# Performance work log

Hardware: AMD Instinct MI355X
Metric: run time of the kernel (lower is better)

The kernel has to match this reference:

```python
import jax, jax.numpy as jnp
import numpy as np

TOPOLOGY = [-1, 0, 0, 0, 1, 2, 3, 4, 5, 6, 7, 8, 9, 9, 9, 12, 13, 14, 16, 17, 18, 19, 20, 21]
JOINT_WEIGHTS = np.ones(24, dtype=np.float32)
B1 = 1.0
B2 = 1.0


def quaternion_to_matrix(q):
    # pytorch3d convention: real part first (w, x, y, z)
    w, x, y, z = q[..., 0], q[..., 1], q[..., 2], q[..., 3]
    two_s = 2.0 / jnp.sum(q * q, axis=-1)
    o = jnp.stack([
        1 - two_s * (y * y + z * z), two_s * (x * y - z * w), two_s * (x * z + y * w),
        two_s * (x * y + z * w), 1 - two_s * (x * x + z * z), two_s * (y * z - x * w),
        two_s * (x * z - y * w), two_s * (y * z + x * w), 1 - two_s * (x * x + y * y),
    ], axis=-1)
    return o.reshape(q.shape[:-1] + (3, 3))


def fk(topology, X_m, X_t):
    # X_m: (bs, T, J*4+3), X_t: (bs, J, 3)
    J = len(topology)
    quat = X_m[..., :-3].reshape(X_m.shape[:-1] + (J, 4))
    local_rot = quaternion_to_matrix(quat)          # (bs, T, J, 3, 3)
    grots = [None] * J
    gtrs = [None] * J
    grots[0] = local_rot[..., 0, :, :]
    gtrs[0] = X_m[..., -3:]                          # root translation
    for i in range(1, J):
        pi = topology[i]
        grots[i] = jnp.matmul(grots[pi], local_rot[..., i, :, :])
        gtrs[i] = jnp.einsum('btij,bj->bti', grots[pi], X_t[:, i]) + gtrs[pi]
    return jnp.stack(grots, axis=-3), jnp.stack(gtrs, axis=-2)


def split_raw_motion(raw_motion):
    position = raw_motion[..., -3:]
    rotation = raw_motion[..., :-3]
    rotation = rotation.reshape(rotation.shape[:-1] + (-1, 4))
    norm = jnp.linalg.norm(rotation, axis=-1, keepdims=True)
    rotation = rotation / jnp.maximum(norm, 1e-12)
    return rotation, position


def weighted_mse(w, a, b):
    # w: (J,), a/b: (bs, T, J, C) -> per-joint weighted mean squared error
    return jnp.mean(w[None, None, :, None] * (a - b) ** 2)


def setup_inputs() -> dict:
    key = jax.random.key(0)
    k1, k2, k3, k4 = jax.random.split(key, 4)
    bs, T, J = 64, 2048, 24
    return {
        'Y_m': jax.random.normal(k1, (bs, T, J * 4 + 3), dtype=jnp.float32),
        'X_m': jax.random.normal(k2, (bs, T, J * 4 + 3), dtype=jnp.float32),
        'Y_t': jax.random.normal(k3, (bs, J, 3), dtype=jnp.float32),
        'X_t': jax.random.normal(k4, (bs, J, 3), dtype=jnp.float32),
    }


def reference(Y_m, X_m, Y_t, X_t):
    w = jnp.asarray(JOINT_WEIGHTS)
    rot_x, pos_x = split_raw_motion(X_m)
    rot_y, pos_y = split_raw_motion(Y_m)
    grot_y, gtr_y = fk(TOPOLOGY, Y_m, Y_t)
    grot_x, gtr_x = fk(TOPOLOGY, X_m, X_t)
    loss_rot = B1 * weighted_mse(w, rot_y, rot_x)
    loss_fk = B2 * (2.5 * weighted_mse(w, gtr_y, gtr_x)
                    + jnp.mean((pos_y - pos_x) ** 2))
    return loss_rot + loss_fk
```

## Files before the change

### kernel.cpp

```cpp
#include <hip/hip_runtime.h>

#define BS 64
#define TT 2048
#define NJ 24
#define ROWF 99
#define BLOCK 64
#define NROWS (BS * TT)
#define LSTR 20

__device__ __forceinline__ float4 ld4u(const float* __restrict__ p) {
  return *reinterpret_cast<const float4*>(p);
}

__device__ __forceinline__ void quat2mat_s(float w, float x, float y, float z,
                                           float s, float* R) {
  const float xx = s*x*x, yy = s*y*y, zz = s*z*z;
  const float xy = s*x*y, xz = s*x*z, yz = s*y*z;
  const float xw = s*x*w, yw = s*y*w, zw = s*z*w;
  R[0] = 1.0f - (yy+zz); R[1] = xy - zw;        R[2] = xz + yw;
  R[3] = xy + zw;        R[4] = 1.0f - (xx+zz); R[5] = yz - xw;
  R[6] = xz - yw;        R[7] = yz + xw;        R[8] = 1.0f - (xx+yy);
}

__device__ __forceinline__ void mm3(const float* A, const float* B, float* C) {
#pragma unroll
  for (int r = 0; r < 3; ++r) {
#pragma unroll
    for (int c = 0; c < 3; ++c) {
      C[3*r+c] = fmaf(A[3*r], B[c], fmaf(A[3*r+1], B[3+c], A[3*r+2]*B[6+c]));
    }
  }
}

__global__ __launch_bounds__(BLOCK, 2) void motion_loss_kernel(
    const float* __restrict__ Ym, const float* __restrict__ Xm,
    const float* __restrict__ Yt, const float* __restrict__ Xt,
    float* __restrict__ out) {
  __shared__ __align__(16) float lX[2][BLOCK * LSTR];
  __shared__ __align__(16) float lY[2][BLOCK * LSTR];

  const int t = threadIdx.x;
  const size_t row0 = (size_t)blockIdx.x * BLOCK;
  const int b = blockIdx.x >> 5;
  const float* __restrict__ xt = Xm + row0 * ROWF;
  const float* __restrict__ yt = Ym + row0 * ROWF;
  const float* __restrict__ tX = Xt + (size_t)b * NJ * 3;
  const float* __restrict__ tY = Yt + (size_t)b * NJ * 3;

  const float4 posx = ld4u(xt + t * ROWF + 95);
  const float4 posy = ld4u(yt + t * ROWF + 95);

  float4 sx[4], sy[4];

#define STAGE_ISSUE(w) do {                                                    \
    _Pragma("unroll")                                                          \
    for (int k = 0; k < 4; ++k) {                                              \
      const int l = t + k * BLOCK, r = l >> 2, s = l & 3;                      \
      sx[k] = ld4u(xt + r * ROWF + (w) * 16 + s * 4);                          \
      sy[k] = ld4u(yt + r * ROWF + (w) * 16 + s * 4);                          \
    }                                                                          \
  } while (0)

#define STAGE_WRITE(w) do {                                                    \
    _Pragma("unroll")                                                          \
    for (int k = 0; k < 4; ++k) {                                              \
      const int l = t + k * BLOCK, r = l >> 2, s = l & 3;                      \
      *reinterpret_cast<float4*>(&lX[(w) & 1][r * LSTR + s * 4]) = sx[k];      \
      *reinterpret_cast<float4*>(&lY[(w) & 1][r * LSTR + s * 4]) = sy[k];      \
    }                                                                          \
  } while (0)

  STAGE_ISSUE(0);
  STAGE_WRITE(0);
  STAGE_ISSUE(1);

  float GX[3][9], GY[3][9], D[3][3];
  float rot_acc = 0.0f, gtr_acc = 0.0f, pos_acc = 0.0f;

  {
    const float4 vx = *reinterpret_cast<const float4*>(&lX[0][t * LSTR]);
    const float4 vy = *reinterpret_cast<const float4*>(&lY[0][t * LSTR]);
    const float qqx = vx.x*vx.x + vx.y*vx.y + vx.z*vx.z + vx.w*vx.w;
    const float qqy = vy.x*vy.x + vy.y*vy.y + vy.z*vy.z + vy.w*vy.w;
    const float ix = rsqrtf(fmaxf(qqx, 1e-24f));
    const float iy = rsqrtf(fmaxf(qqy, 1e-24f));
    const float r0 = vy.x*iy - vx.x*ix, r1 = vy.y*iy - vx.y*ix;
    const float r2 = vy.z*iy - vx.z*ix, r3 = vy.w*iy - vx.w*ix;
    rot_acc += r0*r0 + r1*r1 + r2*r2 + r3*r3;
    quat2mat_s(vx.x, vx.y, vx.z, vx.w, 2.0f*ix*ix, GX[0]);
    quat2mat_s(vy.x, vy.y, vy.z, vy.w, 2.0f*iy*iy, GY[0]);
    D[0][0] = posy.y - posx.y; D[0][1] = posy.z - posx.z; D[0][2] = posy.w - posx.w;
    const float dd = D[0][0]*D[0][0] + D[0][1]*D[0][1] + D[0][2]*D[0][2];
    gtr_acc += dd;
    pos_acc  = dd;
  }

#define JSTEP(j, PS, NS) do {                                                  \
    const float4 vx = *reinterpret_cast<const float4*>(                        \
        &lX[((j) >> 2) & 1][t * LSTR + ((j) & 3) * 4]);                        \
    const float4 vy = *reinterpret_cast<const float4*>(                        \
        &lY[((j) >> 2) & 1][t * LSTR + ((j) & 3) * 4]);                        \
    const float qqx = vx.x*vx.x + vx.y*vx.y + vx.z*vx.z + vx.w*vx.w;           \
    const float qqy = vy.x*vy.x + vy.y*vy.y + vy.z*vy.z + vy.w*vy.w;           \
    const float ix = rsqrtf(fmaxf(qqx, 1e-24f));                               \
    const float iy = rsqrtf(fmaxf(qqy, 1e-24f));                               \
    const float r0 = vy.x*iy - vx.x*ix, r1 = vy.y*iy - vx.y*ix;                \
    const float r2 = vy.z*iy - vx.z*ix, r3 = vy.w*iy - vx.w*ix;                \
    rot_acc += r0*r0 + r1*r1 + r2*r2 + r3*r3;                                  \
    const float tx0 = tX[3*(j)], tx1 = tX[3*(j)+1], tx2 = tX[3*(j)+2];         \
    const float ty0 = tY[3*(j)], ty1 = tY[3*(j)+1], ty2 = tY[3*(j)+2];         \
    const float vx0 = fmaf(GX[PS][0],tx0, fmaf(GX[PS][1],tx1, GX[PS][2]*tx2)); \
    const float vx1 = fmaf(GX[PS][3],tx0, fmaf(GX[PS][4],tx1, GX[PS][5]*tx2)); \
    const float vx2 = fmaf(GX[PS][6],tx0, fmaf(GX[PS][7],tx1, GX[PS][8]*tx2)); \
    const float vy0 = fmaf(GY[PS][0],ty0, fmaf(GY[PS][1],ty1, GY[PS][2]*ty2)); \
    const float vy1 = fmaf(GY[PS][3],ty0, fmaf(GY[PS][4],ty1, GY[PS][5]*ty2)); \
    const float vy2 = fmaf(GY[PS][6],ty0, fmaf(GY[PS][7],ty1, GY[PS][8]*ty2)); \
    const float d0 = D[PS][0] + (vy0 - vx0);                                   \
    const float d1 = D[PS][1] + (vy1 - vx1);                                   \
    const float d2 = D[PS][2] + (vy2 - vx2);                                   \
    gtr_acc += d0*d0 + d1*d1 + d2*d2;                                          \
    float RX[9], RY[9], GnX[9], GnY[9];                                        \
    quat2mat_s(vx.x, vx.y, vx.z, vx.w, 2.0f*ix*ix, RX);                        \
    quat2mat_s(vy.x, vy.y, vy.z, vy.w, 2.0f*iy*iy, RY);                        \
    mm3(GX[PS], RX, GnX);                                                      \
    mm3(GY[PS], RY, GnY);                                                      \
    _Pragma("unroll")                                                          \
    for (int k = 0; k < 9; ++k) { GX[NS][k] = GnX[k]; GY[NS][k] = GnY[k]; }    \
    D[NS][0] = d0; D[NS][1] = d1; D[NS][2] = d2;                               \
  } while (0)

#define BOUNDARY(wnext, wissue) do {                                           \
    STAGE_WRITE(wnext);                                                        \
    if ((wissue) < 6) STAGE_ISSUE(wissue);                                     \
  } while (0)

  JSTEP( 1, 0, 1); JSTEP( 2, 0, 2); JSTEP( 3, 0, 0);
  BOUNDARY(1, 2);
  JSTEP( 4, 1, 1); JSTEP( 5, 2, 2); JSTEP( 6, 0, 0); JSTEP( 7, 1, 1);
  BOUNDARY(2, 3);
  JSTEP( 8, 2, 2); JSTEP( 9, 0, 0); JSTEP(10, 1, 1); JSTEP(11, 2, 2);
  BOUNDARY(3, 4);
  JSTEP(12, 0, 1); JSTEP(13, 0, 2); JSTEP(14, 0, 0); JSTEP(15, 1, 1);
  BOUNDARY(4, 5);
  JSTEP(16, 2, 2); JSTEP(17, 0, 0); JSTEP(18, 2, 2); JSTEP(19, 0, 0);
  BOUNDARY(5, 6);
  JSTEP(20, 2, 2); JSTEP(21, 0, 0); JSTEP(22, 2, 2); JSTEP(23, 0, 0);
#undef JSTEP
#undef BOUNDARY
#undef STAGE_ISSUE
#undef STAGE_WRITE

  const float c_rot = 1.0f / ((float)NROWS * NJ * 4);
  const float c_gtr = 2.5f / ((float)NROWS * NJ * 3);
  const float c_pos = 1.0f / ((float)NROWS * 3);
  float contrib = c_rot * rot_acc + c_gtr * gtr_acc + c_pos * pos_acc;
#pragma unroll
  for (int o = 32; o > 0; o >>= 1) contrib += __shfl_down(contrib, o, 64);
  if (t == 0) atomicAdd(out, contrib);
}

extern "C" void kernel_launch(void* const* d_in, const int* in_sizes, int n_in,
                              void* d_out, int out_size, void* d_ws, size_t ws_size,
                              hipStream_t stream) {
  const float* Ym = (const float*)d_in[0];
  const float* Xm = (const float*)d_in[1];
  const float* Yt = (const float*)d_in[2];
  const float* Xt = (const float*)d_in[3];
  float* out = (float*)d_out;
  hipMemsetAsync(out, 0, sizeof(float), stream);
  motion_loss_kernel<<<NROWS / BLOCK, BLOCK, 0, stream>>>(Ym, Xm, Yt, Xt, out);
}
```

Baseline: 153.3 us.

## Deepen global-load prefetch to two register banks and interleave issues with joint steps

Replaces the single staging register set with two alternating banks (A/B), so each 16-float window is loaded two stages ahead of use rather than one. Loads for the next window are split into per-k chunks placed between individual joint steps to spread memory issue across compute. Per-thread base pointers are precomputed to cut address arithmetic. This raises register pressure (16 extra float4s) under launch_bounds(64,2), which could hurt occupancy or cause spills.

```diff
diff --git a/kernel.cpp b/kernel.cpp
--- a/kernel.cpp
+++ b/kernel.cpp
@@ -50,29 +50,35 @@
   const float4 posx = ld4u(xt + t * ROWF + 95);
   const float4 posy = ld4u(yt + t * ROWF + 95);
 
-  float4 sx[4], sy[4];
+  const float* bx[4]; const float* by[4];
+#pragma unroll
+  for (int k = 0; k < 4; ++k) {
+    const int l = t + k * BLOCK, r = l >> 2, s = l & 3;
+    bx[k] = xt + r * ROWF + s * 4;
+    by[k] = yt + r * ROWF + s * 4;
+  }
 
-#define STAGE_ISSUE(w) do {                                                    \
+  float4 sxA[4], syA[4], sxB[4], syB[4];
+
+#define ISSUE2(w, BX, BY, k) do {                                              \
+    BX[k] = ld4u(bx[k] + (w) * 16);                                            \
+    BY[k] = ld4u(by[k] + (w) * 16);                                            \
+  } while (0)
+
+#define WRITE_BANK(w, BX, BY) do {                                             \
     _Pragma("unroll")                                                          \
     for (int k = 0; k < 4; ++k) {                                              \
       const int l = t + k * BLOCK, r = l >> 2, s = l & 3;                      \
-      sx[k] = ld4u(xt + r * ROWF + (w) * 16 + s * 4);                          \
-      sy[k] = ld4u(yt + r * ROWF + (w) * 16 + s * 4);                          \
+      *reinterpret_cast<float4*>(&lX[(w) & 1][r * LSTR + s * 4]) = BX[k];      \
+      *reinterpret_cast<float4*>(&lY[(w) & 1][r * LSTR + s * 4]) = BY[k];      \
     }                                                                          \
   } while (0)
 
-#define STAGE_WRITE(w) do {                                                    \
-    _Pragma("unroll")                                                          \
-    for (int k = 0; k < 4; ++k) {                                              \
-      const int l = t + k * BLOCK, r = l >> 2, s = l & 3;                      \
-      *reinterpret_cast<float4*>(&lX[(w) & 1][r * LSTR + s * 4]) = sx[k];      \
-      *reinterpret_cast<float4*>(&lY[(w) & 1][r * LSTR + s * 4]) = sy[k];      \
-    }                                                                          \
-  } while (0)
-
-  STAGE_ISSUE(0);
-  STAGE_WRITE(0);
-  STAGE_ISSUE(1);
+  ISSUE2(0, sxA, syA, 0); ISSUE2(0, sxA, syA, 1);
+  ISSUE2(0, sxA, syA, 2); ISSUE2(0, sxA, syA, 3);
+  ISSUE2(1, sxB, syB, 0); ISSUE2(1, sxB, syB, 1);
+  ISSUE2(1, sxB, syB, 2); ISSUE2(1, sxB, syB, 3);
+  WRITE_BANK(0, sxA, syA);
 
   float GX[3][9], GY[3][9], D[3][3];
   float rot_acc = 0.0f, gtr_acc = 0.0f, pos_acc = 0.0f;
@@ -129,26 +135,32 @@
     D[NS][0] = d0; D[NS][1] = d1; D[NS][2] = d2;                               \
   } while (0)
 
-#define BOUNDARY(wnext, wissue) do {                                           \
-    STAGE_WRITE(wnext);                                                        \
-    if ((wissue) < 6) STAGE_ISSUE(wissue);                                     \
-  } while (0)
-
-  JSTEP( 1, 0, 1); JSTEP( 2, 0, 2); JSTEP( 3, 0, 0);
-  BOUNDARY(1, 2);
-  JSTEP( 4, 1, 1); JSTEP( 5, 2, 2); JSTEP( 6, 0, 0); JSTEP( 7, 1, 1);
-  BOUNDARY(2, 3);
-  JSTEP( 8, 2, 2); JSTEP( 9, 0, 0); JSTEP(10, 1, 1); JSTEP(11, 2, 2);
-  BOUNDARY(3, 4);
-  JSTEP(12, 0, 1); JSTEP(13, 0, 2); JSTEP(14, 0, 0); JSTEP(15, 1, 1);
-  BOUNDARY(4, 5);
+        ISSUE2(2, sxA, syA, 0);
+  JSTEP( 1, 0, 1);      ISSUE2(2, sxA, syA, 1);
+  JSTEP( 2, 0, 2);      ISSUE2(2, sxA, syA, 2);
+  JSTEP( 3, 0, 0);      ISSUE2(2, sxA, syA, 3);
+  WRITE_BANK(1, sxB, syB);
+  JSTEP( 4, 1, 1);      ISSUE2(3, sxB, syB, 0);
+  JSTEP( 5, 2, 2);      ISSUE2(3, sxB, syB, 1);
+  JSTEP( 6, 0, 0);      ISSUE2(3, sxB, syB, 2);
+  JSTEP( 7, 1, 1);      ISSUE2(3, sxB, syB, 3);
+  WRITE_BANK(2, sxA, syA);
+  JSTEP( 8, 2, 2);      ISSUE2(4, sxA, syA, 0);
+  JSTEP( 9, 0, 0);      ISSUE2(4, sxA, syA, 1);
+  JSTEP(10, 1, 1);      ISSUE2(4, sxA, syA, 2);
+  JSTEP(11, 2, 2);      ISSUE2(4, sxA, syA, 3);
+  WRITE_BANK(3, sxB, syB);
+  JSTEP(12, 0, 1);      ISSUE2(5, sxB, syB, 0);
+  JSTEP(13, 0, 2);      ISSUE2(5, sxB, syB, 1);
+  JSTEP(14, 0, 0);      ISSUE2(5, sxB, syB, 2);
+  JSTEP(15, 1, 1);      ISSUE2(5, sxB, syB, 3);
+  WRITE_BANK(4, sxA, syA);
   JSTEP(16, 2, 2); JSTEP(17, 0, 0); JSTEP(18, 2, 2); JSTEP(19, 0, 0);
-  BOUNDARY(5, 6);
+  WRITE_BANK(5, sxB, syB);
   JSTEP(20, 2, 2); JSTEP(21, 0, 0); JSTEP(22, 2, 2); JSTEP(23, 0, 0);
 #undef JSTEP
-#undef BOUNDARY
-#undef STAGE_ISSUE
-#undef STAGE_WRITE
+#undef ISSUE2
+#undef WRITE_BANK
 
   const float c_rot = 1.0f / ((float)NROWS * NJ * 4);
   const float c_gtr = 2.5f / ((float)NROWS * NJ * 3);
```

After: 153.3 us. About the same (-0.0%).
